# Optimization experiments

Measured on AMD Instinct MI355X. Metric: run time of the kernel, lower is better.

The kernel has to match this reference:

```python
import jax, jax.numpy as jnp
import numpy as np

HIDDEN = 768
HEAD = 64


def setup_inputs() -> dict:
    key = jax.random.key(0)
    ks = jax.random.split(key, 9)
    s = 1.0 / np.sqrt(HIDDEN)
    so = 1.0 / np.sqrt(HEAD)
    return {
        "x": jax.random.normal(ks[0], (4, 4096, HIDDEN), dtype=jnp.float32),
        "Wq": jax.random.uniform(ks[1], (HIDDEN, HEAD), jnp.float32, -s, s),
        "bq": jax.random.uniform(ks[2], (HEAD,), jnp.float32, -s, s),
        "Wk": jax.random.uniform(ks[3], (HIDDEN, HEAD), jnp.float32, -s, s),
        "bk": jax.random.uniform(ks[4], (HEAD,), jnp.float32, -s, s),
        "Wv": jax.random.uniform(ks[5], (HIDDEN, HEAD), jnp.float32, -s, s),
        "bv": jax.random.uniform(ks[6], (HEAD,), jnp.float32, -s, s),
        "Wo": jax.random.uniform(ks[7], (HEAD, HIDDEN), jnp.float32, -so, so),
        "bo": jax.random.uniform(ks[8], (HIDDEN,), jnp.float32, -so, so),
    }


def reference(x, Wq, bq, Wk, bk, Wv, bv, Wo, bo):
    # x: [b, s, h]
    q = jnp.einsum('bsh,hd->bsd', x, Wq) + bq  # [b, s, d]
    k = jnp.einsum('bsh,hd->bsd', x, Wk) + bk
    v = jnp.einsum('bsh,hd->bsd', x, Wv) + bv
    scale = 1.0 / jnp.sqrt(jnp.asarray(HEAD, x.dtype))
    scores = jnp.einsum('bqd,bkd->bqk', q, k) * scale  # [b, s, s]
    A = jax.nn.softmax(scores, axis=-1)
    ctx = jnp.einsum('bqk,bkd->bqd', A, v)  # [b, s, d]
    return jnp.einsum('bsd,dh->bsh', ctx, Wo) + bo
```

## Files before the change

kernel.cpp:

```cpp
#include <hip/hip_runtime.h>
#include <hip/hip_bf16.h>
#include <stdint.h>

#define BB 4
#define SS 4096
#define HH 768
#define DD 64

typedef __attribute__((ext_vector_type(8))) short bf16x8;
typedef __attribute__((ext_vector_type(4))) short bf16x4;
typedef __attribute__((ext_vector_type(4))) float f32x4;
typedef __attribute__((ext_vector_type(16))) float f32x16;
typedef __attribute__((ext_vector_type(4))) uint32_t u32x4;

__device__ __forceinline__ short f2bf(float f) {
  uint32_t u = __builtin_bit_cast(uint32_t, f);
  u += 0x7fffu + ((u >> 16) & 1u);
  return (short)(u >> 16);
}

#define QSCALE 0.18033688011112042f

__global__ __launch_bounds__(256) void prep_kernel(
    const float* __restrict__ Wq, const float* __restrict__ bq,
    const float* __restrict__ Wk, const float* __restrict__ bk,
    const float* __restrict__ Wv, const float* __restrict__ bv,
    const float* __restrict__ Wo,
    short* __restrict__ wqkvF, float* __restrict__ bqkv,
    short* __restrict__ woF) {
  int idx = blockIdx.x * 256 + threadIdx.x;
  const int N1 = 192 * HH;
  const int N2 = HH * DD;
  if (idx < N1) {
    int n = idx / HH, k = idx % HH;
    float v;
    if (n < 64)       v = Wq[k * 64 + n] * QSCALE;
    else if (n < 128) v = Wk[k * 64 + (n - 64)];
    else              v = Wv[k * 64 + (n - 128)];
    int tile = (n >> 4) * 24 + (k >> 5);
    int lane = (((k >> 3) & 3) << 4) | (n & 15);
    wqkvF[tile * 512 + lane * 8 + (k & 7)] = f2bf(v);
  } else if (idx < N1 + N2) {
    int j = idx - N1;
    int n = j / 64, k = j % 64;
    int tile = (n >> 4) * 2 + (k >> 5);
    int lane = (((k >> 3) & 3) << 4) | (n & 15);
    woF[tile * 512 + lane * 8 + (k & 7)] = f2bf(Wo[k * HH + n]);
  } else if (idx < N1 + N2 + 192) {
    int n = idx - N1 - N2;
    float v;
    if (n < 64)       v = bq[n] * QSCALE;
    else if (n < 128) v = bk[n - 64];
    else              v = bv[n - 128];
    bqkv[n] = v;
  }
}

__global__ __launch_bounds__(256, 2) void qkv_kernel(
    const float* __restrict__ x, const short* __restrict__ wF,
    const float* __restrict__ bqkv,
    short* __restrict__ qb, short* __restrict__ kb, short* __restrict__ vb) {
  __shared__ short xl[32 * 776];
  const int tid = threadIdx.x;
  const int w = tid >> 6, lane = tid & 63, g = (lane >> 4) & 3, n16 = lane & 15;
  const int m0 = blockIdx.x * 32;

  const float4* xsrc = (const float4*)&x[m0 * HH];
#pragma unroll
  for (int i = 0; i < 24; ++i) {
    int idx = i * 256 + tid;
    const float4 f = xsrc[idx];
    int elem = idx * 4;
    int row = elem / HH, col = elem % HH;
    bf16x4 p = { f2bf(f.x), f2bf(f.y), f2bf(f.z), f2bf(f.w) };
    *(bf16x4*)&xl[row * 776 + col] = p;
  }
  __syncthreads();

  f32x4 acc[2][3] = {};
  const short* wbase = &wF[w * 36864 + lane * 8];

#pragma unroll 2
  for (int kc = 0; kc < 24; ++kc) {
    const int ko = kc * 32 + g * 8;
    bf16x8 a0 = *(const bf16x8*)&xl[n16 * 776 + ko];
    bf16x8 a1 = *(const bf16x8*)&xl[(16 + n16) * 776 + ko];
    bf16x8 b0 = *(const bf16x8*)&wbase[kc * 512];
    bf16x8 b1 = *(const bf16x8*)&wbase[12288 + kc * 512];
    bf16x8 b2 = *(const bf16x8*)&wbase[24576 + kc * 512];
    acc[0][0] = __builtin_amdgcn_mfma_f32_16x16x32_bf16(a0, b0, acc[0][0], 0, 0, 0);
    acc[1][0] = __builtin_amdgcn_mfma_f32_16x16x32_bf16(a1, b0, acc[1][0], 0, 0, 0);
    acc[0][1] = __builtin_amdgcn_mfma_f32_16x16x32_bf16(a0, b1, acc[0][1], 0, 0, 0);
    acc[1][1] = __builtin_amdgcn_mfma_f32_16x16x32_bf16(a1, b1, acc[1][1], 0, 0, 0);
    acc[0][2] = __builtin_amdgcn_mfma_f32_16x16x32_bf16(a0, b2, acc[0][2], 0, 0, 0);
    acc[1][2] = __builtin_amdgcn_mfma_f32_16x16x32_bf16(a1, b2, acc[1][2], 0, 0, 0);
  }

#pragma unroll
  for (int ct = 0; ct < 3; ++ct) {
    int nG = w * 48 + ct * 16 + n16;
    float bias = bqkv[nG];
#pragma unroll
    for (int rt = 0; rt < 2; ++rt)
#pragma unroll
      for (int r = 0; r < 4; ++r) {
        int rowg = m0 + rt * 16 + g * 4 + r;
        short val = f2bf(acc[rt][ct][r] + bias);
        if (nG < 64)        qb[rowg * 64 + nG] = val;
        else if (nG < 128)  kb[rowg * 64 + (nG - 64)] = val;
        else                vb[rowg * 64 + (nG - 128)] = val;
      }
  }
}

__global__ __launch_bounds__(256) void vtrans_kernel(
    const short* __restrict__ vb, short* __restrict__ vT) {
  __shared__ short t[64][72];
  const int tid = threadIdx.x;
  const int b = blockIdx.x >> 6, st = blockIdx.x & 63;
  {
    int row = tid >> 2, off = (tid & 3) * 16;
    const short* src = &vb[(b * SS + st * 64 + row) * 64 + off];
    *(bf16x8*)&t[row][off]     = *(const bf16x8*)&src[0];
    *(bf16x8*)&t[row][off + 8] = *(const bf16x8*)&src[8];
  }
  __syncthreads();
  {
    int d = tid >> 2, soff = (tid & 3) * 16;
    bf16x8 o0, o1;
#pragma unroll
    for (int j = 0; j < 8; ++j) o0[j] = t[soff + j][d];
#pragma unroll
    for (int j = 0; j < 8; ++j) o1[j] = t[soff + 8 + j][d];
    short* dst = &vT[(b * 64 + d) * SS + st * 64 + soff];
    *(bf16x8*)&dst[0] = o0;
    *(bf16x8*)&dst[8] = o1;
  }
}

__global__ __launch_bounds__(256, 3) void flash_kernel(
    const short* __restrict__ qb, const short* __restrict__ kb,
    const short* __restrict__ vT,
    float* __restrict__ Opart, float* __restrict__ lpart) {
  __shared__ short Kl[128 * 72];
  __shared__ short Vl[64 * 136];
  __shared__ float l_lds[64];
  const int tid = threadIdx.x;
  const int w = tid >> 6, lane = tid & 63;
  const int m31 = lane & 31, h = lane >> 5;
  const int qt32 = w & 1, kh = w >> 1;
  const int part = blockIdx.x, rg = part >> 2, sp = part & 3;
  const int b = rg >> 6, qt = rg & 63;
  const short* qB = qb + (b * SS + qt * 64 + qt32 * 32) * DD;
  const short* kB = kb + (b * SS + sp * 1024) * DD;
  const short* vB = vT + b * DD * SS + sp * 1024;

  bf16x8 aQ[4];
#pragma unroll
  for (int kk = 0; kk < 4; ++kk)
    aQ[kk] = *(const bf16x8*)&qB[m31 * DD + kk * 16 + 8 * h];

  f32x16 oacc[2] = {};
  float l_run = 0.f;

  for (int kt = 0; kt < 8; ++kt) {
    __syncthreads();
#pragma unroll
    for (int i = 0; i < 4; ++i) {
      int lin = tid + 256 * i;
      int key = lin >> 3, ch = lin & 7;
      *(bf16x8*)&Kl[key * 72 + ch * 8] =
          *(const bf16x8*)&kB[(kt * 128 + key) * DD + ch * 8];
    }
#pragma unroll
    for (int i = 0; i < 4; ++i) {
      int lin = tid + 256 * i;
      int d = lin >> 4, ch = lin & 15;
      *(bf16x8*)&Vl[d * 136 + ch * 8] =
          *(const bf16x8*)&vB[d * SS + kt * 128 + ch * 8];
    }
    __syncthreads();

#pragma unroll
    for (int kt2 = 0; kt2 < 2; ++kt2) {
      f32x16 sc = {};
#pragma unroll
      for (int kk = 0; kk < 4; ++kk) {
        bf16x8 aK = *(const bf16x8*)&Kl[(kh * 64 + kt2 * 32 + m31) * 72 +
                                        kk * 16 + 8 * h];
        sc = __builtin_amdgcn_mfma_f32_32x32x16_bf16(aK, aQ[kk], sc, 0, 0, 0);
      }

      uint32_t pp[8];
      float lsum = 0.f;
#pragma unroll
      for (int j = 0; j < 8; ++j) {
        uint32_t ta = __builtin_bit_cast(uint32_t,
                        __builtin_amdgcn_exp2f(sc[2 * j])) & 0xffff0000u;
        uint32_t tb = __builtin_bit_cast(uint32_t,
                        __builtin_amdgcn_exp2f(sc[2 * j + 1])) & 0xffff0000u;
        lsum += __builtin_bit_cast(float, ta) + __builtin_bit_cast(float, tb);
        pp[j] = (ta >> 16) | tb;
      }
      l_run += lsum;

      uint32_t ee[8];
#pragma unroll
      for (int j = 0; j < 8; ++j)
        ee[j] = (uint32_t)__shfl_xor((int)pp[j], 32);

#pragma unroll
      for (int s = 0; s < 2; ++s) {
        u32x4 fr;
        if (s == 0)
          fr = h ? u32x4{ee[2], ee[3], pp[2], pp[3]}
                 : u32x4{pp[0], pp[1], ee[0], ee[1]};
        else
          fr = h ? u32x4{ee[6], ee[7], pp[6], pp[7]}
                 : u32x4{pp[4], pp[5], ee[4], ee[5]};
        bf16x8 aP = __builtin_bit_cast(bf16x8, fr);
        const int koff = kh * 64 + kt2 * 32 + s * 16 + 8 * h;
#pragma unroll
        for (int dt = 0; dt < 2; ++dt) {
          bf16x8 bV = *(const bf16x8*)&Vl[(dt * 32 + m31) * 136 + koff];
          oacc[dt] = __builtin_amdgcn_mfma_f32_32x32x16_bf16(aP, bV, oacc[dt], 0, 0, 0);
        }
      }
    }
  }

  l_run += __shfl_xor(l_run, 32);

  __syncthreads();
  float* sO = (float*)Kl;
  if (kh == 1) {
#pragma unroll
    for (int dt = 0; dt < 2; ++dt)
#pragma unroll
      for (int r = 0; r < 16; ++r) {
        int q = (r & 3) + 8 * (r >> 2) + 4 * h;
        sO[qt32 * 2048 + q * 64 + dt * 32 + m31] = oacc[dt][r];
      }
    if (lane < 32) l_lds[qt32 * 32 + lane] = l_run;
  }
  __syncthreads();
  if (kh == 0) {
#pragma unroll
    for (int dt = 0; dt < 2; ++dt)
#pragma unroll
      for (int r = 0; r < 16; ++r) {
        int q = (r & 3) + 8 * (r >> 2) + 4 * h;
        float o = oacc[dt][r] + sO[qt32 * 2048 + q * 64 + dt * 32 + m31];
        Opart[(part * 64 + qt32 * 32 + q) * 64 + dt * 32 + m31] = o;
      }
    if (lane < 32)
      lpart[part * 64 + qt32 * 32 + lane] = l_run + l_lds[qt32 * 32 + lane];
  }
}

__global__ __launch_bounds__(256, 4) void proj_kernel(
    const float* __restrict__ Opart, const float* __restrict__ lpart,
    const short* __restrict__ woF, const float* __restrict__ bo,
    float* __restrict__ out) {
  const int tid = threadIdx.x;
  const int w = tid >> 6, lane = tid & 63, g = lane >> 4, n16 = lane & 15;
  const int m0 = blockIdx.x * 16;
  const int colbase = w * 192;

  const int row = m0 + n16;
  const int rg = row >> 6, r64 = row & 63;
  float lsum = lpart[(rg * 4 + 0) * 64 + r64] + lpart[(rg * 4 + 1) * 64 + r64] +
               lpart[(rg * 4 + 2) * 64 + r64] + lpart[(rg * 4 + 3) * 64 + r64];
  float inv = 1.f / lsum;

  bf16x8 aC[2];
#pragma unroll
  for (int kk = 0; kk < 2; ++kk) {
    const int d0 = kk * 32 + g * 8;
    float s0 = 0, s1 = 0, s2 = 0, s3 = 0, s4 = 0, s5 = 0, s6 = 0, s7 = 0;
#pragma unroll
    for (int sp = 0; sp < 4; ++sp) {
      const float* op = &Opart[((rg * 4 + sp) * 64 + r64) * 64 + d0];
      const float4 v0 = *(const float4*)&op[0];
      const float4 v1 = *(const float4*)&op[4];
      s0 += v0.x; s1 += v0.y; s2 += v0.z; s3 += v0.w;
      s4 += v1.x; s5 += v1.y; s6 += v1.z; s7 += v1.w;
    }
    aC[kk] = bf16x8{ f2bf(s0 * inv), f2bf(s1 * inv), f2bf(s2 * inv), f2bf(s3 * inv),
                     f2bf(s4 * inv), f2bf(s5 * inv), f2bf(s6 * inv), f2bf(s7 * inv) };
  }

  const short* wbase = &woF[w * 12288 + lane * 8];

  f32x4 acc[12] = {};
#pragma unroll
  for (int kk = 0; kk < 2; ++kk) {
#pragma unroll
    for (int ct = 0; ct < 12; ++ct) {
      bf16x8 bW = *(const bf16x8*)&wbase[(ct * 2 + kk) * 512];
      acc[ct] = __builtin_amdgcn_mfma_f32_16x16x32_bf16(aC[kk], bW, acc[ct], 0, 0, 0);
    }
  }
#pragma unroll
  for (int ct = 0; ct < 12; ++ct) {
    int nG = colbase + ct * 16 + n16;
    float bias = bo[nG];
#pragma unroll
    for (int r = 0; r < 4; ++r) {
      int rowg = m0 + g * 4 + r;
      out[rowg * HH + nG] = acc[ct][r] + bias;
    }
  }
}

extern "C" void kernel_launch(void* const* d_in, const int* in_sizes, int n_in,
                              void* d_out, int out_size, void* d_ws, size_t ws_size,
                              hipStream_t stream) {
  const float* x  = (const float*)d_in[0];
  const float* Wq = (const float*)d_in[1];
  const float* bq = (const float*)d_in[2];
  const float* Wk = (const float*)d_in[3];
  const float* bk = (const float*)d_in[4];
  const float* Wv = (const float*)d_in[5];
  const float* bv = (const float*)d_in[6];
  const float* Wo = (const float*)d_in[7];
  const float* bo = (const float*)d_in[8];
  float* out = (float*)d_out;

  char* ws = (char*)d_ws;
  short* qb    = (short*)(ws + 0);
  short* kb    = (short*)(ws + (2u << 20));
  short* vb    = (short*)(ws + (4u << 20));
  short* vT    = (short*)(ws + (6u << 20));
  short* wqkvF = (short*)(ws + (8u << 20));
  short* woF   = (short*)(ws + (8u << 20) + 384 * 1024);
  float* bqkv  = (float*)(ws + (8u << 20) + 512 * 1024);
  float* lpart = (float*)(ws + (9u << 20));
  float* Opart = (float*)(ws + (10u << 20));

  hipLaunchKernelGGL(prep_kernel, dim3(769), dim3(256), 0, stream,
                     Wq, bq, Wk, bk, Wv, bv, Wo, wqkvF, bqkv, woF);
  hipLaunchKernelGGL(qkv_kernel, dim3(512), dim3(256), 0, stream,
                     x, wqkvF, bqkv, qb, kb, vb);
  hipLaunchKernelGGL(vtrans_kernel, dim3(256), dim3(256), 0, stream,
                     vb, vT);
  hipLaunchKernelGGL(flash_kernel, dim3(1024), dim3(256), 0, stream,
                     qb, kb, vT, Opart, lpart);
  hipLaunchKernelGGL(proj_kernel, dim3(1024), dim3(256), 0, stream,
                     Opart, lpart, woF, bo, out);
}
```

Before: 170.0 us.

## Emit MFMA-fragment Q/K/V layouts and drop LDS staging in flash kernel

The QKV kernel now stages its outputs through LDS and writes Q, K and V directly in the MFMA operand-fragment order. This makes the separate V-transpose kernel unnecessary. The flash kernel drops its K/V LDS tiles and barriers: each wave owns 32 queries and reads K/V fragments straight from global memory, and the key range is split 8 ways instead of 4. The projection kernel reduces the 8 partials. In exchange, the four waves of a block no longer share K/V loads through LDS and the partial output buffer grows, adding global and cache traffic.

```diff
diff --git a/kernel.cpp b/kernel.cpp
--- a/kernel.cpp
+++ b/kernel.cpp
@@ -59,7 +59,7 @@
 __global__ __launch_bounds__(256, 2) void qkv_kernel(
     const float* __restrict__ x, const short* __restrict__ wF,
     const float* __restrict__ bqkv,
-    short* __restrict__ qb, short* __restrict__ kb, short* __restrict__ vb) {
+    short* __restrict__ qF, short* __restrict__ kF, short* __restrict__ vF) {
   __shared__ short xl[32 * 776];
   const int tid = threadIdx.x;
   const int w = tid >> 6, lane = tid & 63, g = (lane >> 4) & 3, n16 = lane & 15;
@@ -96,166 +96,119 @@
     acc[1][2] = __builtin_amdgcn_mfma_f32_16x16x32_bf16(a1, b2, acc[1][2], 0, 0, 0);
   }
 
+  __syncthreads();
+  short* sh = xl;
 #pragma unroll
   for (int ct = 0; ct < 3; ++ct) {
-    int nG = w * 48 + ct * 16 + n16;
-    float bias = bqkv[nG];
+    int col = w * 48 + ct * 16 + n16;
+    float bias = bqkv[col];
 #pragma unroll
     for (int rt = 0; rt < 2; ++rt)
 #pragma unroll
-      for (int r = 0; r < 4; ++r) {
-        int rowg = m0 + rt * 16 + g * 4 + r;
-        short val = f2bf(acc[rt][ct][r] + bias);
-        if (nG < 64)        qb[rowg * 64 + nG] = val;
-        else if (nG < 128)  kb[rowg * 64 + (nG - 64)] = val;
-        else                vb[rowg * 64 + (nG - 128)] = val;
-      }
-  }
-}
-
-__global__ __launch_bounds__(256) void vtrans_kernel(
-    const short* __restrict__ vb, short* __restrict__ vT) {
-  __shared__ short t[64][72];
-  const int tid = threadIdx.x;
-  const int b = blockIdx.x >> 6, st = blockIdx.x & 63;
+      for (int r = 0; r < 4; ++r)
+        sh[(rt * 16 + g * 4 + r) * 200 + col] = f2bf(acc[rt][ct][r] + bias);
+  }
+  __syncthreads();
+
   {
-    int row = tid >> 2, off = (tid & 3) * 16;
-    const short* src = &vb[(b * SS + st * 64 + row) * 64 + off];
-    *(bf16x8*)&t[row][off]     = *(const bf16x8*)&src[0];
-    *(bf16x8*)&t[row][off + 8] = *(const bf16x8*)&src[8];
-  }
-  __syncthreads();
+    int kkh = tid >> 5, m31k = tid & 31;
+    bf16x8 qv = *(const bf16x8*)&sh[m31k * 200 + kkh * 8];
+    bf16x8 kv = *(const bf16x8*)&sh[m31k * 200 + 64 + kkh * 8];
+    *(bf16x8*)&qF[m0 * 64 + tid * 8] = qv;
+    *(bf16x8*)&kF[m0 * 64 + tid * 8] = kv;
+  }
   {
-    int d = tid >> 2, soff = (tid & 3) * 16;
-    bf16x8 o0, o1;
-#pragma unroll
-    for (int j = 0; j < 8; ++j) o0[j] = t[soff + j][d];
-#pragma unroll
-    for (int j = 0; j < 8; ++j) o1[j] = t[soff + 8 + j][d];
-    short* dst = &vT[(b * 64 + d) * SS + st * 64 + soff];
-    *(bf16x8*)&dst[0] = o0;
-    *(bf16x8*)&dst[8] = o1;
-  }
-}
-
-__global__ __launch_bounds__(256, 3) void flash_kernel(
-    const short* __restrict__ qb, const short* __restrict__ kb,
-    const short* __restrict__ vT,
+    int d = tid & 63, g8i = tid >> 6;
+    bf16x8 vv;
+#pragma unroll
+    for (int j = 0; j < 8; ++j) vv[j] = sh[(g8i * 8 + j) * 200 + 128 + d];
+    int b0 = m0 >> 12, s0b = m0 & 4095;
+    *(bf16x8*)&vF[b0 * 262144 + s0b * 64 + tid * 8] = vv;
+  }
+}
+
+__global__ __launch_bounds__(256, 2) void flash_kernel(
+    const short* __restrict__ qF, const short* __restrict__ kF,
+    const short* __restrict__ vF,
     float* __restrict__ Opart, float* __restrict__ lpart) {
-  __shared__ short Kl[128 * 72];
-  __shared__ short Vl[64 * 136];
-  __shared__ float l_lds[64];
   const int tid = threadIdx.x;
   const int w = tid >> 6, lane = tid & 63;
   const int m31 = lane & 31, h = lane >> 5;
-  const int qt32 = w & 1, kh = w >> 1;
-  const int part = blockIdx.x, rg = part >> 2, sp = part & 3;
-  const int b = rg >> 6, qt = rg & 63;
-  const short* qB = qb + (b * SS + qt * 64 + qt32 * 32) * DD;
-  const short* kB = kb + (b * SS + sp * 1024) * DD;
-  const short* vB = vT + b * DD * SS + sp * 1024;
-
+  const int idx = blockIdx.x;
+  const int sp = idx & 7, qg = (idx >> 3) & 31, b = idx >> 8;
+  const int qs = qg * 4 + w;
+  const int laneoff = h * 256 + m31 * 8;
+
+  const short* qbase = qF + (b * 128 + qs) * 2048 + laneoff;
   bf16x8 aQ[4];
 #pragma unroll
   for (int kk = 0; kk < 4; ++kk)
-    aQ[kk] = *(const bf16x8*)&qB[m31 * DD + kk * 16 + 8 * h];
-
+    aQ[kk] = *(const bf16x8*)&qbase[kk * 512];
+
+  const short* vFb = vF + b * 262144 + m31 * 8;
   f32x16 oacc[2] = {};
   float l_run = 0.f;
 
-  for (int kt = 0; kt < 8; ++kt) {
-    __syncthreads();
-#pragma unroll
-    for (int i = 0; i < 4; ++i) {
-      int lin = tid + 256 * i;
-      int key = lin >> 3, ch = lin & 7;
-      *(bf16x8*)&Kl[key * 72 + ch * 8] =
-          *(const bf16x8*)&kB[(kt * 128 + key) * DD + ch * 8];
-    }
-#pragma unroll
-    for (int i = 0; i < 4; ++i) {
-      int lin = tid + 256 * i;
-      int d = lin >> 4, ch = lin & 15;
-      *(bf16x8*)&Vl[d * 136 + ch * 8] =
-          *(const bf16x8*)&vB[d * SS + kt * 128 + ch * 8];
-    }
-    __syncthreads();
-
-#pragma unroll
-    for (int kt2 = 0; kt2 < 2; ++kt2) {
-      f32x16 sc = {};
-#pragma unroll
-      for (int kk = 0; kk < 4; ++kk) {
-        bf16x8 aK = *(const bf16x8*)&Kl[(kh * 64 + kt2 * 32 + m31) * 72 +
-                                        kk * 16 + 8 * h];
-        sc = __builtin_amdgcn_mfma_f32_32x32x16_bf16(aK, aQ[kk], sc, 0, 0, 0);
+#pragma unroll 2
+  for (int kt2 = 0; kt2 < 16; ++kt2) {
+    const int kt = sp * 16 + kt2;
+    const short* kbase = kF + (b * 128 + kt) * 2048 + laneoff;
+
+    f32x16 sc = {};
+#pragma unroll
+    for (int kk = 0; kk < 4; ++kk) {
+      bf16x8 aK = *(const bf16x8*)&kbase[kk * 512];
+      sc = __builtin_amdgcn_mfma_f32_32x32x16_bf16(aK, aQ[kk], sc, 0, 0, 0);
+    }
+
+    uint32_t pp[8];
+    float lsum = 0.f;
+#pragma unroll
+    for (int j = 0; j < 8; ++j) {
+      uint32_t ta = __builtin_bit_cast(uint32_t,
+                      __builtin_amdgcn_exp2f(sc[2 * j])) & 0xffff0000u;
+      uint32_t tb = __builtin_bit_cast(uint32_t,
+                      __builtin_amdgcn_exp2f(sc[2 * j + 1])) & 0xffff0000u;
+      lsum += __builtin_bit_cast(float, ta) + __builtin_bit_cast(float, tb);
+      pp[j] = (ta >> 16) | tb;
+    }
+    l_run += lsum;
+
+    uint32_t ee[8];
+#pragma unroll
+    for (int j = 0; j < 8; ++j)
+      ee[j] = (uint32_t)__shfl_xor((int)pp[j], 32);
+
+    const short* vtile = vFb + (kt * 4 + h) * 512;
+#pragma unroll
+    for (int s = 0; s < 2; ++s) {
+      u32x4 fr;
+      if (s == 0)
+        fr = h ? u32x4{ee[2], ee[3], pp[2], pp[3]}
+               : u32x4{pp[0], pp[1], ee[0], ee[1]};
+      else
+        fr = h ? u32x4{ee[6], ee[7], pp[6], pp[7]}
+               : u32x4{pp[4], pp[5], ee[4], ee[5]};
+      bf16x8 aP = __builtin_bit_cast(bf16x8, fr);
+#pragma unroll
+      for (int dt = 0; dt < 2; ++dt) {
+        bf16x8 bV = *(const bf16x8*)&vtile[s * 1024 + dt * 256];
+        oacc[dt] = __builtin_amdgcn_mfma_f32_32x32x16_bf16(aP, bV, oacc[dt], 0, 0, 0);
       }
-
-      uint32_t pp[8];
-      float lsum = 0.f;
-#pragma unroll
-      for (int j = 0; j < 8; ++j) {
-        uint32_t ta = __builtin_bit_cast(uint32_t,
-                        __builtin_amdgcn_exp2f(sc[2 * j])) & 0xffff0000u;
-        uint32_t tb = __builtin_bit_cast(uint32_t,
-                        __builtin_amdgcn_exp2f(sc[2 * j + 1])) & 0xffff0000u;
-        lsum += __builtin_bit_cast(float, ta) + __builtin_bit_cast(float, tb);
-        pp[j] = (ta >> 16) | tb;
-      }
-      l_run += lsum;
-
-      uint32_t ee[8];
-#pragma unroll
-      for (int j = 0; j < 8; ++j)
-        ee[j] = (uint32_t)__shfl_xor((int)pp[j], 32);
-
-#pragma unroll
-      for (int s = 0; s < 2; ++s) {
-        u32x4 fr;
-        if (s == 0)
-          fr = h ? u32x4{ee[2], ee[3], pp[2], pp[3]}
-                 : u32x4{pp[0], pp[1], ee[0], ee[1]};
-        else
-          fr = h ? u32x4{ee[6], ee[7], pp[6], pp[7]}
-                 : u32x4{pp[4], pp[5], ee[4], ee[5]};
-        bf16x8 aP = __builtin_bit_cast(bf16x8, fr);
-        const int koff = kh * 64 + kt2 * 32 + s * 16 + 8 * h;
-#pragma unroll
-        for (int dt = 0; dt < 2; ++dt) {
-          bf16x8 bV = *(const bf16x8*)&Vl[(dt * 32 + m31) * 136 + koff];
-          oacc[dt] = __builtin_amdgcn_mfma_f32_32x32x16_bf16(aP, bV, oacc[dt], 0, 0, 0);
-        }
-      }
     }
   }
 
   l_run += __shfl_xor(l_run, 32);
 
-  __syncthreads();
-  float* sO = (float*)Kl;
-  if (kh == 1) {
-#pragma unroll
-    for (int dt = 0; dt < 2; ++dt)
-#pragma unroll
-      for (int r = 0; r < 16; ++r) {
-        int q = (r & 3) + 8 * (r >> 2) + 4 * h;
-        sO[qt32 * 2048 + q * 64 + dt * 32 + m31] = oacc[dt][r];
-      }
-    if (lane < 32) l_lds[qt32 * 32 + lane] = l_run;
-  }
-  __syncthreads();
-  if (kh == 0) {
-#pragma unroll
-    for (int dt = 0; dt < 2; ++dt)
-#pragma unroll
-      for (int r = 0; r < 16; ++r) {
-        int q = (r & 3) + 8 * (r >> 2) + 4 * h;
-        float o = oacc[dt][r] + sO[qt32 * 2048 + q * 64 + dt * 32 + m31];
-        Opart[(part * 64 + qt32 * 32 + q) * 64 + dt * 32 + m31] = o;
-      }
-    if (lane < 32)
-      lpart[part * 64 + qt32 * 32 + lane] = l_run + l_lds[qt32 * 32 + lane];
-  }
+  const int part = (b * 128 + qs) * 8 + sp;
+#pragma unroll
+  for (int dt = 0; dt < 2; ++dt)
+#pragma unroll
+    for (int r = 0; r < 16; ++r) {
+      int q = (r & 3) + 8 * (r >> 2) + 4 * h;
+      Opart[(part * 32 + q) * 64 + dt * 32 + m31] = oacc[dt][r];
+    }
+  if (lane < 32) lpart[part * 32 + lane] = l_run;
 }
 
 __global__ __launch_bounds__(256, 4) void proj_kernel(
@@ -267,10 +220,11 @@
   const int m0 = blockIdx.x * 16;
   const int colbase = w * 192;
 
-  const int row = m0 + n16;
-  const int rg = row >> 6, r64 = row & 63;
-  float lsum = lpart[(rg * 4 + 0) * 64 + r64] + lpart[(rg * 4 + 1) * 64 + r64] +
-               lpart[(rg * 4 + 2) * 64 + r64] + lpart[(rg * 4 + 3) * 64 + r64];
+  const int q = m0 + n16;
+  const int pg = q >> 5, q31 = q & 31;
+  float lsum = 0.f;
+#pragma unroll
+  for (int sp = 0; sp < 8; ++sp) lsum += lpart[(pg * 8 + sp) * 32 + q31];
   float inv = 1.f / lsum;
 
   bf16x8 aC[2];
@@ -279,8 +233,8 @@
     const int d0 = kk * 32 + g * 8;
     float s0 = 0, s1 = 0, s2 = 0, s3 = 0, s4 = 0, s5 = 0, s6 = 0, s7 = 0;
 #pragma unroll
-    for (int sp = 0; sp < 4; ++sp) {
-      const float* op = &Opart[((rg * 4 + sp) * 64 + r64) * 64 + d0];
+    for (int sp = 0; sp < 8; ++sp) {
+      const float* op = &Opart[((pg * 8 + sp) * 32 + q31) * 64 + d0];
       const float4 v0 = *(const float4*)&op[0];
       const float4 v1 = *(const float4*)&op[4];
       s0 += v0.x; s1 += v0.y; s2 += v0.z; s3 += v0.w;
@@ -328,24 +282,21 @@
   float* out = (float*)d_out;
 
   char* ws = (char*)d_ws;
-  short* qb    = (short*)(ws + 0);
-  short* kb    = (short*)(ws + (2u << 20));
-  short* vb    = (short*)(ws + (4u << 20));
-  short* vT    = (short*)(ws + (6u << 20));
-  short* wqkvF = (short*)(ws + (8u << 20));
-  short* woF   = (short*)(ws + (8u << 20) + 384 * 1024);
-  float* bqkv  = (float*)(ws + (8u << 20) + 512 * 1024);
-  float* lpart = (float*)(ws + (9u << 20));
-  float* Opart = (float*)(ws + (10u << 20));
+  short* qF    = (short*)(ws + 0);
+  short* kF    = (short*)(ws + (2u << 20));
+  short* vF    = (short*)(ws + (4u << 20));
+  short* wqkvF = (short*)(ws + (6u << 20));
+  short* woF   = (short*)(ws + (6u << 20) + 384 * 1024);
+  float* bqkv  = (float*)(ws + (6u << 20) + 512 * 1024);
+  float* lpart = (float*)(ws + (7u << 20));
+  float* Opart = (float*)(ws + (8u << 20));
 
   hipLaunchKernelGGL(prep_kernel, dim3(769), dim3(256), 0, stream,
                      Wq, bq, Wk, bk, Wv, bv, Wo, wqkvF, bqkv, woF);
   hipLaunchKernelGGL(qkv_kernel, dim3(512), dim3(256), 0, stream,
-                     x, wqkvF, bqkv, qb, kb, vb);
-  hipLaunchKernelGGL(vtrans_kernel, dim3(256), dim3(256), 0, stream,
-                     vb, vT);
+                     x, wqkvF, bqkv, qF, kF, vF);
   hipLaunchKernelGGL(flash_kernel, dim3(1024), dim3(256), 0, stream,
-                     qb, kb, vT, Opart, lpart);
+                     qF, kF, vF, Opart, lpart);
   hipLaunchKernelGGL(proj_kernel, dim3(1024), dim3(256), 0, stream,
                      Opart, lpart, woF, bo, out);
 }
```

Result: slower. 178.5 us (+5.0%).
